# Optimization experiments

Hardware: AMD Instinct MI355X
Metric: run time of the kernel (lower is better)

The kernel has to match this reference:

```python
import jax, jax.numpy as jnp
import numpy as np

MASK_NUM = float(-2**32 + 1)  # additive masking constant from the original module


def setup_inputs() -> dict:
    key = jax.random.key(0)
    kq, kk, kv, km = jax.random.split(key, 4)
    BH, S, D = 32, 2048, 64   # batch*heads, seq_len, head_dim
    B = 4                     # true batch (masks leading dim)
    queries = jax.random.normal(kq, (BH, S, D), dtype=jnp.float32)
    keys = jax.random.normal(kk, (BH, S, D), dtype=jnp.float32)
    values = jax.random.normal(kv, (BH, S, D), dtype=jnp.float32)
    masks = jax.random.randint(km, (B, S), 0, 2, dtype=jnp.int32)  # 1 = masked key
    return {"queries": queries, "keys": keys, "values": values, "masks": masks}


def reference(queries, keys, values, masks):
    d = queries.shape[-1]
    # QK^T, scaled by sqrt(d): [BH, Sq, Sk]
    scores = jnp.einsum('bqd,bkd->bqk', queries, keys) / (d ** 0.5)
    # key-padding mask: tile [B, Sk] -> [BH, Sk], additive large negative
    heads = queries.shape[0] // masks.shape[0]
    m = jnp.tile(masks.astype(jnp.float32), (heads, 1))[:, None, :]  # [BH,1,Sk]
    scores = scores + m * MASK_NUM
    # causal (future) mask: replace upper-triangular entries with MASK_NUM
    Sq, Sk = scores.shape[1], scores.shape[2]
    tril = jnp.tril(jnp.ones((Sq, Sk), dtype=scores.dtype))
    scores = jnp.where(tril == 0, MASK_NUM, scores)
    attn = jax.nn.softmax(scores, axis=-1)
    # dropout_rate = 0.0 -> identity
    return jnp.einsum('bqk,bkd->bqd', attn, values)
```

## Files before the change

kernel.cpp:

```cpp
#include <hip/hip_runtime.h>
#include <hip/hip_bf16.h>

#define S_LEN  2048
#define DHEAD  64
#define NHEADS 32
#define NBATCH 4
#define LOG2E  1.44269504f
#define CMASK  (-4294967296.0f * 1.44269504f)

typedef __attribute__((ext_vector_type(4)))  float f4;
typedef __attribute__((ext_vector_type(8)))  short bh8;
typedef __attribute__((ext_vector_type(16))) float f16x;
typedef __attribute__((ext_vector_type(4)))  int   i4;
typedef __attribute__((ext_vector_type(2)))  int   i2;
typedef unsigned short ushort_t;

static __device__ __forceinline__ unsigned short f2b(float f){
    unsigned int x = __builtin_bit_cast(unsigned int, f);
    x += 0x7FFFu + ((x >> 16) & 1u);
    return (unsigned short)(x >> 16);
}
static __device__ __forceinline__ float b2f(ushort_t u){
    return __builtin_bit_cast(float, ((unsigned)u) << 16);
}
static __device__ __forceinline__ int cvtpk(float a, float b){
    int r; asm("v_cvt_pk_bf16_f32 %0, %1, %2" : "=v"(r) : "v"(a), "v"(b)); return r;
}

__global__ __launch_bounds__(256)
void prep(const float* __restrict__ K, const float* __restrict__ V,
          const int* __restrict__ M,
          ushort_t* __restrict__ Kb, ushort_t* __restrict__ Vt,
          float* __restrict__ colpart, unsigned* __restrict__ mbits)
{
    const int bid = blockIdx.x;
    const int tid = threadIdx.x;
    if (bid < 2048){
        const int i = bid * 256 + tid;
        const f4* p = (const f4*)(K + (size_t)i * 8);
        f4 a = p[0], b = p[1];
        bh8 w;
        #pragma unroll
        for (int k = 0; k < 4; ++k){ w[k] = (short)f2b(a[k]); w[k+4] = (short)f2b(b[k]); }
        *(bh8*)(Kb + (size_t)i * 8) = w;
    } else if (bid < 3072){
        __shared__ short T[64][72];
        __shared__ float red[64][4];
        const int r2 = bid - 2048;
        const int head = r2 >> 5;
        const int kv0  = (r2 & 31) * 64;
        {
            const int r = tid >> 2;
            const int s = (tid & 3) * 16;
            const float* vp = V + ((size_t)head * S_LEN + kv0 + r) * DHEAD + s;
            f4 v0 = *(const f4*)(vp);
            f4 v1 = *(const f4*)(vp + 4);
            f4 v2 = *(const f4*)(vp + 8);
            f4 v3 = *(const f4*)(vp + 12);
            float vv[16];
            *(f4*)&vv[0] = v0; *(f4*)&vv[4] = v1; *(f4*)&vv[8] = v2; *(f4*)&vv[12] = v3;
            #pragma unroll
            for (int i = 0; i < 16; ++i) T[r][s + i] = (short)f2b(vv[i]);
        }
        __syncthreads();
        {
            const int d  = tid >> 2;
            const int k0 = (tid & 3) * 16;
            bh8 w0, w1;
            float s16 = 0.f;
            #pragma unroll
            for (int i = 0; i < 8; ++i){
                w0[i] = T[k0 + i][d];
                w1[i] = T[k0 + 8 + i][d];
                s16 += b2f((ushort_t)w0[i]) + b2f((ushort_t)w1[i]);
            }
            ushort_t* op = Vt + ((size_t)head * DHEAD + d) * S_LEN + kv0 + k0;
            *(bh8*)op       = w0;
            *(bh8*)(op + 8) = w1;
            red[d][tid & 3] = s16;
        }
        __syncthreads();
        if (tid < 64)
            colpart[(size_t)r2 * 64 + tid] =
                red[tid][0] + red[tid][1] + red[tid][2] + red[tid][3];
    } else {
        const int* mp = M + ((size_t)(tid >> 6) << 11) + ((tid & 63) << 5);
        unsigned bits = 0u;
        #pragma unroll
        for (int j = 0; j < 32; j += 4){
            i4 v = *(const i4*)(mp + j);
            bits |= (v[0] != 0 ? (1u << j) : 0u) | (v[1] != 0 ? (2u << j) : 0u)
                  | (v[2] != 0 ? (4u << j) : 0u) | (v[3] != 0 ? (8u << j) : 0u);
        }
        mbits[tid] = bits;
    }
}

__global__ __launch_bounds__(256, 2)
void attn_main(const float* __restrict__ Q, const ushort_t* __restrict__ Kb,
               const ushort_t* __restrict__ Vt, const unsigned* __restrict__ mbits,
               ushort_t* __restrict__ Obuf, float* __restrict__ mlbuf)
{
    __shared__ char SMEM[2][16384];

    const int tid  = threadIdx.x;
    const int wave = tid >> 6;
    const int lane = tid & 63;
    const int lq   = lane & 31;
    const int hi   = lane >> 5;

    const int bid  = blockIdx.x;
    const int head = ((bid & 7) << 2) | ((bid >> 3) & 3);
    const int c    = bid >> 5;
    const int s    = c & 1;
    const int j    = 15 - (c >> 1);
    const int b    = head & (NBATCH - 1);
    const size_t hoff = (size_t)head * S_LEN * DHEAD;

    const int q0w = (j << 7) + (wave << 5);
    const int dq  = q0w + lq;
    const int td  = q0w >> 6;
    const int kt0 = s * (j + 1);
    const int ntb = j + 1;

    const ushort_t* kbase = Kb + hoff;
    const ushort_t* vbase = Vt + (size_t)head * DHEAD * S_LEN;

    const int mwords = __builtin_bit_cast(int, mbits[(b << 6) + lane]);

    bh8 qB[4];
    {
        const float* qp = Q + hoff + (size_t)(q0w + lq) * DHEAD;
        const float qs = 0.125f * LOG2E;
        #pragma unroll
        for (int ks = 0; ks < 4; ++ks){
            f4 f0 = *(const f4*)(qp + ks * 16 + hi * 8);
            f4 f1 = *(const f4*)(qp + ks * 16 + hi * 8 + 4);
            bh8 aa;
            #pragma unroll
            for (int i = 0; i < 4; ++i){
                aa[i]   = (short)f2b(f0[i] * qs);
                aa[i+4] = (short)f2b(f1[i] * qs);
            }
            qB[ks] = aa;
        }
    }

    auto stage = [&](int buf, int kv0){
        #pragma unroll
        for (int i = 0; i < 2; ++i){
            const int o   = ((i << 8) + tid) << 4;
            const int row = o >> 7;
            const int cb  = (o & 127) ^ ((row & 7) << 4);
            const char* ks = (const char*)kbase + (size_t)(kv0 + row) * 128 + cb;
            const char* vs = (const char*)vbase + (size_t)row * (S_LEN * 2)
                             + (size_t)kv0 * 2 + cb;
            __builtin_amdgcn_global_load_lds(
                (const __attribute__((address_space(1))) void*)ks,
                (__attribute__((address_space(3))) void*)(&SMEM[buf][o]), 16, 0, 0);
            __builtin_amdgcn_global_load_lds(
                (const __attribute__((address_space(1))) void*)vs,
                (__attribute__((address_space(3))) void*)(&SMEM[buf][8192 + o]), 16, 0, 0);
        }
    };

    f16x acc0 = {};
    f16x acc1 = {};
    float m = -INFINITY, l = 0.f;

    stage(0, kt0 << 6);
    asm volatile("s_waitcnt vmcnt(0)" ::: "memory");
    __syncthreads();

    for (int i = 0; i < ntb; ++i){
        const int cur = i & 1;
        const int kt  = kt0 + i;
        if (i + 1 < ntb) stage(cur ^ 1, (kt + 1) << 6);

        if (kt <= td){
            const int kv0 = kt << 6;
            const char* kb = &SMEM[cur][0];
            const char* vb = &SMEM[cur][8192];

            bh8 kf[8];
            #pragma unroll
            for (int t32 = 0; t32 < 2; ++t32)
                #pragma unroll
                for (int ks = 0; ks < 4; ++ks){
                    const int rl = (t32 << 5) + lq;
                    const int cb = ((ks << 5) + (hi << 4)) ^ ((rl & 7) << 4);
                    kf[t32*4+ks] = *(const bh8*)(kb + (rl << 7) + cb);
                }

            f16x s0 = {}, s1 = {};
            __builtin_amdgcn_s_setprio(1);
            #pragma unroll
            for (int ks = 0; ks < 4; ++ks)
                s0 = __builtin_amdgcn_mfma_f32_32x32x16_bf16(kf[ks],   qB[ks], s0, 0, 0, 0);
            #pragma unroll
            for (int ks = 0; ks < 4; ++ks)
                s1 = __builtin_amdgcn_mfma_f32_32x32x16_bf16(kf[4+ks], qB[ks], s1, 0, 0, 0);
            __builtin_amdgcn_s_setprio(0);

            bh8 vf[8];
            #pragma unroll
            for (int aa = 0; aa < 2; ++aa)
                #pragma unroll
                for (int j4 = 0; j4 < 4; ++j4){
                    const int rl = (aa << 5) + lq;
                    const int cb = ((j4 << 5) + (hi << 4)) ^ ((rl & 7) << 4);
                    vf[aa*4+j4] = *(const bh8*)(vb + (rl << 7) + cb);
                }

            const unsigned ml0 = ((unsigned)__builtin_amdgcn_readlane(mwords, 2*kt    )) >> (hi << 2);
            const unsigned ml1 = ((unsigned)__builtin_amdgcn_readlane(mwords, 2*kt + 1)) >> (hi << 2);
            #pragma unroll
            for (int g = 0; g < 4; ++g)
                #pragma unroll
                for (int i2_ = 0; i2_ < 4; ++i2_){
                    s0[g*4+i2_] = ((ml0 >> (g*8+i2_)) & 1u) ? CMASK : s0[g*4+i2_];
                    s1[g*4+i2_] = ((ml1 >> (g*8+i2_)) & 1u) ? CMASK : s1[g*4+i2_];
                }
            if (kt == td){
                #pragma unroll
                for (int g = 0; g < 4; ++g)
                    #pragma unroll
                    for (int i2_ = 0; i2_ < 4; ++i2_){
                        const int k0i = kv0 + (g << 3) + (hi << 2) + i2_;
                        s0[g*4+i2_] = (k0i      > dq) ? CMASK : s0[g*4+i2_];
                        s1[g*4+i2_] = (k0i + 32 > dq) ? CMASK : s1[g*4+i2_];
                    }
            }

            float t8[8];
            #pragma unroll
            for (int i2_ = 0; i2_ < 8; ++i2_)
                t8[i2_] = fmaxf(fmaxf(s0[i2_], s0[i2_+8]), fmaxf(s1[i2_], s1[i2_+8]));
            #pragma unroll
            for (int i2_ = 0; i2_ < 4; ++i2_) t8[i2_] = fmaxf(t8[i2_], t8[i2_+4]);
            float pml = fmaxf(fmaxf(t8[0], t8[1]), fmaxf(t8[2], t8[3]));
            float pm  = fmaxf(pml, __shfl_xor(pml, 32, 64));

            if (!__all(pm <= m + 11.0f)){
                float mn = fmaxf(m, pm);
                float al = __builtin_amdgcn_exp2f(m - mn);
                m = mn;
                l *= al;
                #pragma unroll
                for (int i2_ = 0; i2_ < 16; ++i2_){ acc0[i2_] *= al; acc1[i2_] *= al; }
            }

            #pragma unroll
            for (int i2_ = 0; i2_ < 16; ++i2_){
                s0[i2_] = __builtin_amdgcn_exp2f(s0[i2_] - m);
                s1[i2_] = __builtin_amdgcn_exp2f(s1[i2_] - m);
            }
            float u8[8];
            #pragma unroll
            for (int i2_ = 0; i2_ < 8; ++i2_) u8[i2_] = (s0[i2_] + s0[i2_+8]) + (s1[i2_] + s1[i2_+8]);
            #pragma unroll
            for (int i2_ = 0; i2_ < 4; ++i2_) u8[i2_] = u8[i2_] + u8[i2_+4];
            float lsl = (u8[0] + u8[1]) + (u8[2] + u8[3]);
            l += lsl + __shfl_xor(lsl, 32, 64);

            bh8 pa[4];
            #pragma unroll
            for (int half = 0; half < 2; ++half){
                const f16x& sv = half ? s1 : s0;
                int D[8];
                #pragma unroll
                for (int g = 0; g < 4; ++g){
                    D[2*g]   = cvtpk(sv[4*g],   sv[4*g+1]);
                    D[2*g+1] = cvtpk(sv[4*g+2], sv[4*g+3]);
                }
                int sA0 = hi ? D[0] : D[2],  sA1 = hi ? D[1] : D[3];
                int sB0 = hi ? D[4] : D[6],  sB1 = hi ? D[5] : D[7];
                int rA0 = __shfl_xor(sA0, 32, 64), rA1 = __shfl_xor(sA1, 32, 64);
                int rB0 = __shfl_xor(sB0, 32, 64), rB1 = __shfl_xor(sB1, 32, 64);
                i4 p0 = { hi ? rA0 : D[0], hi ? rA1 : D[1],
                          hi ? D[2] : rA0, hi ? D[3] : rA1 };
                i4 p1 = { hi ? rB0 : D[4], hi ? rB1 : D[5],
                          hi ? D[6] : rB0, hi ? D[7] : rB1 };
                pa[half*2]     = __builtin_bit_cast(bh8, p0);
                pa[half*2 + 1] = __builtin_bit_cast(bh8, p1);
            }

            __builtin_amdgcn_s_setprio(1);
            #pragma unroll
            for (int j4 = 0; j4 < 4; ++j4){
                acc0 = __builtin_amdgcn_mfma_f32_32x32x16_bf16(vf[j4],   pa[j4], acc0, 0, 0, 0);
                acc1 = __builtin_amdgcn_mfma_f32_32x32x16_bf16(vf[4+j4], pa[j4], acc1, 0, 0, 0);
            }
            __builtin_amdgcn_s_setprio(0);
        }

        asm volatile("s_waitcnt vmcnt(0)" ::: "memory");
        __syncthreads();
    }

    ushort_t* ob = Obuf + (((size_t)(s * NHEADS + head) * S_LEN + q0w + lq) << 6);
    #pragma unroll
    for (int g = 0; g < 4; ++g){
        i2 w0, w1;
        w0[0] = cvtpk(acc0[4*g],   acc0[4*g+1]);
        w0[1] = cvtpk(acc0[4*g+2], acc0[4*g+3]);
        w1[0] = cvtpk(acc1[4*g],   acc1[4*g+1]);
        w1[1] = cvtpk(acc1[4*g+2], acc1[4*g+3]);
        *(i2*)((char*)ob + 16*g + 8*hi)      = w0;
        *(i2*)((char*)ob + 64 + 16*g + 8*hi) = w1;
    }
    if (hi == 0){
        float* mlp = mlbuf + (((size_t)(s * NHEADS + head) * S_LEN + q0w + lq) << 1);
        mlp[0] = m;
        mlp[1] = l;
    }
}

__global__ __launch_bounds__(256)
void attn_merge(const ushort_t* __restrict__ Obuf, const float* __restrict__ mlbuf,
                float* __restrict__ Out)
{
    const int gid  = blockIdx.x * 256 + threadIdx.x;
    const int row  = gid >> 2;
    const int part = gid & 3;
    const float* ml0 = mlbuf + ((size_t)row << 1);
    const float* ml1 = mlbuf + (((size_t)(NHEADS * S_LEN) + row) << 1);
    const float m0 = ml0[0], l0 = ml0[1];
    const float m1 = ml1[0], l1 = ml1[1];
    const float ms = fmaxf(m0, m1);
    const float a0 = __builtin_amdgcn_exp2f(m0 - ms);
    const float a1 = __builtin_amdgcn_exp2f(m1 - ms);
    const float inv = 1.0f / (a0 * l0 + a1 * l1);
    const ushort_t* o0 = Obuf + ((size_t)row << 6) + part * 16;
    const ushort_t* o1 = o0 + ((size_t)(NHEADS * S_LEN) << 6);
    bh8 x0a = *(const bh8*)(o0), x0b = *(const bh8*)(o0 + 8);
    bh8 x1a = *(const bh8*)(o1), x1b = *(const bh8*)(o1 + 8);
    float* op = Out + ((size_t)row << 6) + part * 16;
    #pragma unroll
    for (int i = 0; i < 8; ++i){
        op[i]     = (a0 * b2f((ushort_t)x0a[i]) + a1 * b2f((ushort_t)x1a[i])) * inv;
        op[8 + i] = (a0 * b2f((ushort_t)x0b[i]) + a1 * b2f((ushort_t)x1b[i])) * inv;
    }
}

__global__ __launch_bounds__(256)
void attn_fixup(const float* __restrict__ colpart, const int* __restrict__ M,
                float* __restrict__ Out)
{
    __shared__ float red[4][64];
    __shared__ int qstar;
    const int head = blockIdx.x;
    const int b = head & (NBATCH - 1);
    const int tid = threadIdx.x;
    const int col = tid & 63;
    const int grp = tid >> 6;
    {
        float s = 0.f;
        const float* cp = colpart + ((size_t)head * 32 + grp * 8) * 64 + col;
        #pragma unroll
        for (int j = 0; j < 8; ++j) s += cp[j * 64];
        red[grp][col] = s;
    }
    if (tid == 0){
        int q = 0;
        const int* mp = M + (size_t)b * S_LEN;
        while (q < S_LEN && mp[q]) ++q;
        qstar = q;
    }
    __syncthreads();
    const int qs = qstar;
    if (qs == 0) return;
    const float mean = (red[0][col] + red[1][col] + red[2][col] + red[3][col])
                       * (1.0f / S_LEN);
    for (int q = grp; q < qs; q += 4)
        Out[((size_t)head * S_LEN + q) * DHEAD + col] = mean;
}

extern "C" void kernel_launch(void* const* d_in, const int* in_sizes, int n_in,
                              void* d_out, int out_size, void* d_ws, size_t ws_size,
                              hipStream_t stream)
{
    const float* Q = (const float*)d_in[0];
    const float* K = (const float*)d_in[1];
    const float* V = (const float*)d_in[2];
    const int*   M = (const int*)d_in[3];
    float* Out = (float*)d_out;

    ushort_t* Kb = (ushort_t*)d_ws;
    ushort_t* Vt = Kb + (size_t)NHEADS * S_LEN * DHEAD;
    float* colpart = (float*)(Vt + (size_t)NHEADS * S_LEN * DHEAD);
    unsigned* mbits = (unsigned*)(colpart + 1024 * 64);
    ushort_t* Obuf = (ushort_t*)(mbits + 256);
    float* mlbuf = (float*)(Obuf + ((size_t)2 * NHEADS * S_LEN * DHEAD));

    prep      <<<dim3(3073),   dim3(256), 0, stream>>>(K, V, M, Kb, Vt, colpart, mbits);
    attn_main <<<dim3(1024),   dim3(256), 0, stream>>>(Q, Kb, Vt, mbits, Obuf, mlbuf);
    attn_merge<<<dim3(1024),   dim3(256), 0, stream>>>(Obuf, mlbuf, Out);
    attn_fixup<<<dim3(NHEADS), dim3(256), 0, stream>>>(colpart, M, Out);
}
```

Baseline: 64.89 us.

## Generalize split-KV attention to four key splits when workspace allows

Templates the main attention and merge kernels on the number of key-range splits and picks four splits (2048 blocks) when the workspace is large enough, falling back to two. Key tiles per query block are spread evenly across splits, and splits with no tiles skip staging. The aim is more parallelism and shorter per-block work on the causal triangle. The cost is extra partial-output writes and a heavier merge pass, and some splits may do little work for early query blocks.

```diff
diff --git a/kernel.cpp b/kernel.cpp
--- a/kernel.cpp
+++ b/kernel.cpp
@@ -96,6 +96,7 @@
     }
 }
 
+template<int NS>
 __global__ __launch_bounds__(256, 2)
 void attn_main(const float* __restrict__ Q, const ushort_t* __restrict__ Kb,
                const ushort_t* __restrict__ Vt, const unsigned* __restrict__ mbits,
@@ -112,16 +113,18 @@
     const int bid  = blockIdx.x;
     const int head = ((bid & 7) << 2) | ((bid >> 3) & 3);
     const int c    = bid >> 5;
-    const int s    = c & 1;
-    const int j    = 15 - (c >> 1);
+    const int s    = c % NS;
+    const int j    = 15 - (c / NS);
     const int b    = head & (NBATCH - 1);
     const size_t hoff = (size_t)head * S_LEN * DHEAD;
 
     const int q0w = (j << 7) + (wave << 5);
     const int dq  = q0w + lq;
     const int td  = q0w >> 6;
-    const int kt0 = s * (j + 1);
-    const int ntb = j + 1;
+    const int ntk = (j << 1) + 2;
+    const int qn  = ntk / NS, r = ntk % NS;
+    const int kt0 = s * qn + (s < r ? s : r);
+    const int ntb = qn + (s < r ? 1 : 0);
 
     const ushort_t* kbase = Kb + hoff;
     const ushort_t* vbase = Vt + (size_t)head * DHEAD * S_LEN;
@@ -168,9 +171,11 @@
     f16x acc1 = {};
     float m = -INFINITY, l = 0.f;
 
-    stage(0, kt0 << 6);
-    asm volatile("s_waitcnt vmcnt(0)" ::: "memory");
-    __syncthreads();
+    if (ntb > 0){
+        stage(0, kt0 << 6);
+        asm volatile("s_waitcnt vmcnt(0)" ::: "memory");
+        __syncthreads();
+    }
 
     for (int i = 0; i < ntb; ++i){
         const int cur = i & 1;
@@ -316,6 +321,7 @@
     }
 }
 
+template<int NS>
 __global__ __launch_bounds__(256)
 void attn_merge(const ushort_t* __restrict__ Obuf, const float* __restrict__ mlbuf,
                 float* __restrict__ Out)
@@ -323,23 +329,37 @@
     const int gid  = blockIdx.x * 256 + threadIdx.x;
     const int row  = gid >> 2;
     const int part = gid & 3;
-    const float* ml0 = mlbuf + ((size_t)row << 1);
-    const float* ml1 = mlbuf + (((size_t)(NHEADS * S_LEN) + row) << 1);
-    const float m0 = ml0[0], l0 = ml0[1];
-    const float m1 = ml1[0], l1 = ml1[1];
-    const float ms = fmaxf(m0, m1);
-    const float a0 = __builtin_amdgcn_exp2f(m0 - ms);
-    const float a1 = __builtin_amdgcn_exp2f(m1 - ms);
-    const float inv = 1.0f / (a0 * l0 + a1 * l1);
-    const ushort_t* o0 = Obuf + ((size_t)row << 6) + part * 16;
-    const ushort_t* o1 = o0 + ((size_t)(NHEADS * S_LEN) << 6);
-    bh8 x0a = *(const bh8*)(o0), x0b = *(const bh8*)(o0 + 8);
-    bh8 x1a = *(const bh8*)(o1), x1b = *(const bh8*)(o1 + 8);
+    float mv[NS], lv[NS];
+    float ms = -INFINITY;
+    #pragma unroll
+    for (int s = 0; s < NS; ++s){
+        const float* ml = mlbuf + (((size_t)s * (NHEADS * S_LEN) + row) << 1);
+        mv[s] = ml[0]; lv[s] = ml[1];
+        ms = fmaxf(ms, mv[s]);
+    }
+    float av[NS], denom = 0.f;
+    #pragma unroll
+    for (int s = 0; s < NS; ++s){
+        av[s] = __builtin_amdgcn_exp2f(mv[s] - ms);
+        denom += av[s] * lv[s];
+    }
+    const float inv = 1.0f / denom;
+    float oa[8] = {}, ob[8] = {};
+    #pragma unroll
+    for (int s = 0; s < NS; ++s){
+        const ushort_t* o = Obuf + (((size_t)s * (NHEADS * S_LEN) + row) << 6) + part * 16;
+        bh8 xa = *(const bh8*)(o), xb = *(const bh8*)(o + 8);
+        #pragma unroll
+        for (int i = 0; i < 8; ++i){
+            oa[i] += av[s] * b2f((ushort_t)xa[i]);
+            ob[i] += av[s] * b2f((ushort_t)xb[i]);
+        }
+    }
     float* op = Out + ((size_t)row << 6) + part * 16;
     #pragma unroll
     for (int i = 0; i < 8; ++i){
-        op[i]     = (a0 * b2f((ushort_t)x0a[i]) + a1 * b2f((ushort_t)x1a[i])) * inv;
-        op[8 + i] = (a0 * b2f((ushort_t)x0b[i]) + a1 * b2f((ushort_t)x1b[i])) * inv;
+        op[i]     = oa[i] * inv;
+        op[8 + i] = ob[i] * inv;
     }
 }
 
@@ -391,10 +411,19 @@
     float* colpart = (float*)(Vt + (size_t)NHEADS * S_LEN * DHEAD);
     unsigned* mbits = (unsigned*)(colpart + 1024 * 64);
     ushort_t* Obuf = (ushort_t*)(mbits + 256);
-    float* mlbuf = (float*)(Obuf + ((size_t)2 * NHEADS * S_LEN * DHEAD));
-
-    prep      <<<dim3(3073),   dim3(256), 0, stream>>>(K, V, M, Kb, Vt, colpart, mbits);
-    attn_main <<<dim3(1024),   dim3(256), 0, stream>>>(Q, Kb, Vt, mbits, Obuf, mlbuf);
-    attn_merge<<<dim3(1024),   dim3(256), 0, stream>>>(Obuf, mlbuf, Out);
+    const size_t oslice = (size_t)NHEADS * S_LEN * DHEAD;
+    const size_t base = (char*)(Obuf) - (char*)d_ws;
+    const size_t perslice = oslice * 2 + (size_t)NHEADS * S_LEN * 2 * 4;
+    const int NS = (ws_size >= base + 4 * perslice) ? 4 : 2;
+    float* mlbuf = (float*)(Obuf + (size_t)NS * oslice);
+
+    prep<<<dim3(3073), dim3(256), 0, stream>>>(K, V, M, Kb, Vt, colpart, mbits);
+    if (NS == 4){
+        attn_main<4><<<dim3(2048), dim3(256), 0, stream>>>(Q, Kb, Vt, mbits, Obuf, mlbuf);
+        attn_merge<4><<<dim3(1024), dim3(256), 0, stream>>>(Obuf, mlbuf, Out);
+    } else {
+        attn_main<2><<<dim3(1024), dim3(256), 0, stream>>>(Q, Kb, Vt, mbits, Obuf, mlbuf);
+        attn_merge<2><<<dim3(1024), dim3(256), 0, stream>>>(Obuf, mlbuf, Out);
+    }
     attn_fixup<<<dim3(NHEADS), dim3(256), 0, stream>>>(colpart, M, Out);
 }
```

Result: slower. 67.98 us (+4.8%).
